# Kernel tuning notes

Hardware: AMD Instinct MI355X
Metric: run time of the kernel (lower is better)

The kernel has to match this reference:

```python
import math
import jax
import jax.numpy as jnp
import numpy as np

N_ATOMS = 5000
N_EDGES = 100000
FEAT = 128
BERN_K = 16
R_CUT = 5.0
EPS = 1e-15


def _swish(x, a, b):
    # learnable swish: alpha * x * sigmoid(beta * x)
    return a * x * jax.nn.sigmoid(b * x)


def _y_all(r_ij, r, l):
    """Real spherical harmonics of the unit vector r_ij/r, all m in [-l, l]."""
    x, y, z = r_ij[:, 0], r_ij[:, 1], r_ij[:, 2]
    if l == 0:
        return jnp.ones((r_ij.shape[0], 1), r_ij.dtype)
    if l == 1:
        return jnp.stack([y, z, x], axis=1) / r
    s3 = math.sqrt(3.0)
    r2 = (r * r)[:, 0]
    return jnp.stack(
        [s3 * x * y, s3 * y * z, 1.5 * z * z - 0.5 * r2, s3 * x * z, 0.5 * s3 * (x * x - y * y)],
        axis=1,
    ) / r2[:, None]


def _rho_k(r, gamma, K):
    """Bernstein radial basis b_{k,K-1}(exp(-gamma r)) times SpookyNet smooth cutoff."""
    rr = r[:, 0]
    g = jnp.maximum(gamma, 0.0)  # gamma.clamp(0)
    e = jnp.exp(-g * rr)[:, None]  # [E,1]
    k = jnp.arange(K)
    binom = jnp.asarray([math.comb(K - 1, i) for i in range(K)], dtype=r.dtype)
    bern = binom * e ** k * (1.0 - e) ** (K - 1 - k)  # [E,K]
    safe = jnp.where(rr < R_CUT, (R_CUT - rr) * (R_CUT + rr), 1.0)
    fcut = jnp.where(rr < R_CUT, jnp.exp(-rr * rr / safe), 0.0)
    return bern * fcut[:, None]


def _forward(xyz, x_tilde, rm_W1, rm_b1, rm_W2, rm_b2, rm_W3, rm_b3,
             rl_W1, rl_b1, rl_W2, rl_b2, rl_W3, rl_b3,
             G_s, G_p, G_d, P_1, P_2, D_1, D_2,
             gamma_s, gamma_p, gamma_d, sw_alpha, sw_beta, nbrs):
    n = xyz.shape[0]
    sw = lambda t, i: _swish(t, sw_alpha[i], sw_beta[i])
    # batched pre-activation linear over channel dim c
    bl = lambda W, b, t: jnp.einsum('cij,cnj->cni', W, t) + b[:, None, :]

    # BatchedResidualMLP on x_tilde repeated over 4 channels
    x4 = jnp.broadcast_to(x_tilde, (4,) + x_tilde.shape)  # [4,N,F]
    h = x4 + bl(rm_W2, rm_b2, sw(bl(rm_W1, rm_b1, sw(x4, 0)), 1))
    res_outs = x4 + bl(rm_W3, rm_b3, sw(h, 2))  # [4,N,F]

    i0, i1 = nbrs[:, 0], nbrs[:, 1]
    r_ij = xyz[i1] - xyz[i0]  # [E,3]
    r = jnp.sqrt((r_ij ** 2 + EPS).sum(-1, keepdims=True))  # stable norm, [E,1]
    K = G_s.shape[1]

    def quant(l, gamma, G, res_out):
        # g: [E,K,2l+1] = rho_k outer y_lm
        g = _rho_k(r, gamma, K)[:, :, None] * _y_all(r_ij, r, l)[:, None, :]
        mm = jnp.einsum('fk,ekm->efm', G, g)  # [E,F,2l+1]
        per = res_out[i1][:, :, None] * mm
        return jax.ops.segment_sum(per, i0, num_segments=n)  # scatter_add -> [N,F,2l+1]

    q_s = quant(0, gamma_s, G_s, res_outs[1])
    q_p = quant(1, gamma_p, G_p, res_outs[2])
    q_d = quant(2, gamma_d, G_d, res_outs[3])

    def inner(q, M1, M2):
        t1 = jnp.einsum('ij,njm->nim', M1, q)
        t2 = jnp.einsum('ij,njm->nim', M2, q)
        return (t1 * t2).sum(-1)

    inp = res_outs[0] + q_s[:, :, 0] + inner(q_p, P_1, P_2) + inner(q_d, D_1, D_2)

    # ResidualMLP (note: no outer skip, matching the torch code)
    lin = lambda W, b, t: t @ W.T + b
    h2 = inp + lin(rl_W2, rl_b2, sw(lin(rl_W1, rl_b1, sw(inp, 3)), 4))
    return lin(rl_W3, rl_b3, sw(h2, 5))


def setup_inputs():
    key = jax.random.key(0)
    ks = jax.random.split(key, 24)
    p = lambda k, shape: jax.random.normal(k, shape, dtype=jnp.float32) * 0.1
    F, K = FEAT, BERN_K
    return {
        'xyz': jax.random.normal(ks[0], (N_ATOMS, 3), jnp.float32) * 3.0,
        'x_tilde': jax.random.normal(ks[1], (N_ATOMS, F), jnp.float32),
        'nbrs': jax.random.randint(ks[2], (N_EDGES, 2), 0, N_ATOMS),
        'rm_W1': p(ks[3], (4, F, F)), 'rm_b1': p(ks[4], (4, F)),
        'rm_W2': p(ks[5], (4, F, F)), 'rm_b2': p(ks[6], (4, F)),
        'rm_W3': p(ks[7], (4, F, F)), 'rm_b3': p(ks[8], (4, F)),
        'rl_W1': p(ks[9], (F, F)), 'rl_b1': p(ks[10], (F,)),
        'rl_W2': p(ks[11], (F, F)), 'rl_b2': p(ks[12], (F,)),
        'rl_W3': p(ks[13], (F, F)), 'rl_b3': p(ks[14], (F,)),
        'G_s': p(ks[15], (F, K)), 'G_p': p(ks[16], (F, K)), 'G_d': p(ks[17], (F, K)),
        'P_1': p(ks[18], (F, F)), 'P_2': p(ks[19], (F, F)),
        'D_1': p(ks[20], (F, F)), 'D_2': p(ks[21], (F, F)),
        'gamma_s': jnp.asarray(0.5, jnp.float32),
        'gamma_p': jnp.asarray(0.5, jnp.float32),
        'gamma_d': jnp.asarray(0.5, jnp.float32),
        'sw_alpha': jnp.ones((6,), jnp.float32),
        'sw_beta': jnp.full((6,), 1.702, jnp.float32),
    }


def reference(xyz, x_tilde, nbrs, rm_W1, rm_b1, rm_W2, rm_b2, rm_W3, rm_b3,
              rl_W1, rl_b1, rl_W2, rl_b2, rl_W3, rl_b3,
              G_s, G_p, G_d, P_1, P_2, D_1, D_2,
              gamma_s, gamma_p, gamma_d, sw_alpha, sw_beta):
    return _forward(xyz, x_tilde, rm_W1, rm_b1, rm_W2, rm_b2, rm_W3, rm_b3,
                    rl_W1, rl_b1, rl_W2, rl_b2, rl_W3, rl_b3,
                    G_s, G_p, G_d, P_1, P_2, D_1, D_2,
                    gamma_s, gamma_p, gamma_d, sw_alpha, sw_beta, nbrs)
```

## Files before the change

### kernel.cpp

```cpp
#include <hip/hip_runtime.h>
#include <hip/hip_bf16.h>
#include <math.h>

#define NA 5000
#define NE 100000
#define F 128
#define KB 16
#define RCUT 5.0f
#define RECW 28
#define QCAP 40

typedef long long i64;
typedef __attribute__((ext_vector_type(8))) short bf16x8;
typedef __attribute__((ext_vector_type(4))) float f32x4;

__device__ __forceinline__ float swish_f(float t, float a, float b){
    return a * t / (1.0f + __expf(-b * t));
}
__device__ __forceinline__ float bf2f(unsigned short u){
    return __uint_as_float(((unsigned)u) << 16);
}
__device__ __forceinline__ unsigned short f2bf(float x){
    unsigned b = __float_as_uint(x);
    return (unsigned short)((b + 0x8000u) >> 16);
}
__device__ __forceinline__ unsigned pack2(float a, float b){
    return (unsigned)f2bf(a) | ((unsigned)f2bf(b) << 16);
}
__device__ __forceinline__ int swz(int row, int byte_in_row){
    return row * 256 + (byte_in_row ^ ((row & 7) << 4));
}

template<int MT>
__device__ __forceinline__ void gemm_stage(const unsigned short* __restrict__ Wb,
                                           const short* act_lds, f32x4 (&acc)[MT][2],
                                           int lane, int wave)
{
    bf16x8 B[2][4], A[MT][4];
    const int cl = lane & 15, kh = lane >> 4;
    #pragma unroll
    for (int ntl = 0; ntl < 2; ++ntl){
        const unsigned short* wp = Wb + (i64)(wave * 32 + ntl * 16 + cl) * F + kh * 8;
        #pragma unroll
        for (int kb = 0; kb < 4; ++kb)
            B[ntl][kb] = *(const bf16x8*)(wp + kb * 32);
    }
    #pragma unroll
    for (int mt = 0; mt < MT; ++mt){
        int row = mt * 16 + cl;
        #pragma unroll
        for (int kb = 0; kb < 4; ++kb)
            A[mt][kb] = *(const bf16x8*)((const char*)act_lds + swz(row, kb * 64 + kh * 16));
    }
    #pragma unroll
    for (int mt = 0; mt < MT; ++mt)
        #pragma unroll
        for (int ntl = 0; ntl < 2; ++ntl)
            #pragma unroll
            for (int kb = 0; kb < 4; ++kb)
                acc[mt][ntl] = __builtin_amdgcn_mfma_f32_16x16x32_bf16(
                    A[mt][kb], B[ntl][kb], acc[mt][ntl], 0, 0, 0);
}

__device__ __forceinline__ void epi_lds(f32x4 acc[2][2], const float* __restrict__ bc,
                                        const float* resid_lds, int use_resid,
                                        float aS, float bS, short* act_lds,
                                        int lane, int wave)
{
    const int cl = lane & 15, r4 = (lane >> 4) * 4;
    #pragma unroll
    for (int ntl = 0; ntl < 2; ++ntl){
        int col = wave * 32 + ntl * 16 + cl;
        float bv = bc[col];
        #pragma unroll
        for (int mt = 0; mt < 2; ++mt){
            #pragma unroll
            for (int j = 0; j < 4; ++j){
                int row = mt * 16 + r4 + j;
                float z = acc[mt][ntl][j] + bv;
                if (use_resid) z += resid_lds[row * 132 + col];
                z = swish_f(z, aS, bS);
                *(short*)((char*)act_lds + swz(row, col * 2)) = (short)f2bf(z);
            }
        }
    }
}

__device__ __forceinline__ void basis16(float r, float g, float fcut, float* b){
    const float C[KB] = {1.f,15.f,105.f,455.f,1365.f,3003.f,5005.f,6435.f,
                         6435.f,5005.f,3003.f,1365.f,455.f,105.f,15.f,1.f};
    float e = __expf(-fmaxf(g, 0.f) * r);
    float one = 1.f - e;
    float ep = 1.f;
    #pragma unroll
    for (int k = 0; k < KB; ++k){ b[k] = C[k] * ep * fcut; ep *= e; }
    float op = 1.f;
    #pragma unroll
    for (int k = KB-1; k >= 0; --k){ b[k] *= op; op *= one; }
}

__device__ __forceinline__ void prep_edge_block(
    int ebid, const float* __restrict__ xyz, const int* __restrict__ nbrs,
    int* __restrict__ fill, int* __restrict__ idx,
    const float* __restrict__ gs, const float* __restrict__ gp,
    const float* __restrict__ gd, float* __restrict__ rec)
{
    int e = ebid * 256 + threadIdx.x;
    if (e >= NE) return;
    int i0 = nbrs[2*e], i1 = nbrs[2*e+1];
    float dx = xyz[3*i1]   - xyz[3*i0];
    float dy = xyz[3*i1+1] - xyz[3*i0+1];
    float dz = xyz[3*i1+2] - xyz[3*i0+2];
    float r2 = dx*dx + dy*dy + dz*dz + 3e-15f;
    float r = sqrtf(r2);
    if (r >= RCUT) return;
    int slot = atomicAdd(&fill[i0], 1);
    if (slot < QCAP) idx[i0 * QCAP + slot] = e;
    float* R = rec + (i64)e * RECW;
    float ir = 1.f / r;
    R[0] = __int_as_float(i1);
    R[1] = dx * ir; R[2] = dy * ir; R[3] = dz * ir;
    float fcut = __expf(-r2 / ((RCUT - r) * (RCUT + r)));
    float bs[KB], bp[KB], bd[KB];
    basis16(r, gs[0], fcut, bs);
    basis16(r, gp[0], fcut, bp);
    basis16(r, gd[0], fcut, bd);
    unsigned* RW = (unsigned*)(R + 4);
    #pragma unroll
    for (int k = 0; k < 8; ++k) RW[k]      = pack2(bs[2*k], bs[2*k+1]);
    #pragma unroll
    for (int k = 0; k < 8; ++k) RW[8 + k]  = pack2(bp[2*k], bp[2*k+1]);
    #pragma unroll
    for (int k = 0; k < 8; ++k) RW[16 + k] = pack2(bd[2*k], bd[2*k+1]);
}

template<int S0, int S1, int S2, int ADD2, int ADD3, int ADDPART, int PREP, int CH, int RESB>
__global__ __launch_bounds__(256)
void mlp3_mfma(const float* __restrict__ in, const unsigned short* __restrict__ part,
               const unsigned short* __restrict__ W1b, const float* __restrict__ b1,
               const unsigned short* __restrict__ W2b, const float* __restrict__ b2,
               const unsigned short* __restrict__ W3b, const float* __restrict__ b3,
               float* __restrict__ out, unsigned short* __restrict__ resb,
               const float* __restrict__ sw_a, const float* __restrict__ sw_b, int n,
               const float* __restrict__ xyz, const int* __restrict__ nbrs,
               int* __restrict__ fill, int* __restrict__ idx,
               const float* __restrict__ gs, const float* __restrict__ gp,
               const float* __restrict__ gd, float* __restrict__ rec)
{
    if (PREP && blockIdx.y >= CH){
        int ebid = (blockIdx.y - CH) * gridDim.x + blockIdx.x;
        if (ebid < (NE + 255) / 256)
            prep_edge_block(ebid, xyz, nbrs, fill, idx, gs, gp, gd, rec);
        return;
    }

    __shared__ short act_lds[32 * 128];
    __shared__ float resid_lds[32 * 132];
    const int tid = threadIdx.x;
    const int lane = tid & 63, wave = tid >> 6;
    const int c = blockIdx.y;
    const int a0 = blockIdx.x * 32;
    const i64 S = (i64)NA * F;

    const unsigned short* Wc1 = W1b + (i64)c * F * F;
    const unsigned short* Wc2 = W2b + (i64)c * F * F;
    const unsigned short* Wc3 = W3b + (i64)c * F * F;
    const float* bc1 = b1 + c * F;
    const float* bc2 = b2 + c * F;
    const float* bc3 = b3 + c * F;

    {
        float aS = sw_a[S0], bS = sw_b[S0];
        #pragma unroll
        for (int it = 0; it < 4; ++it){
            int ch = tid + it * 256;
            int row = ch >> 5, j4 = ch & 31;
            int g = a0 + row;
            float4 v = make_float4(0.f, 0.f, 0.f, 0.f);
            if (g < n){
                v = *(const float4*)(in + (i64)g * F + j4 * 4);
                if (ADDPART){
                    #pragma unroll
                    for (int m = 0; m < 8; ++m){
                        ushort4 u = *(const ushort4*)(part + (i64)m * S + (i64)g * F + j4 * 4);
                        v.x += bf2f(u.x); v.y += bf2f(u.y);
                        v.z += bf2f(u.z); v.w += bf2f(u.w);
                    }
                }
            }
            *(float4*)&resid_lds[row * 132 + j4 * 4] = v;
            uint2 p;
            p.x = pack2(swish_f(v.x, aS, bS), swish_f(v.y, aS, bS));
            p.y = pack2(swish_f(v.z, aS, bS), swish_f(v.w, aS, bS));
            *(uint2*)((char*)act_lds + swz(row, j4 * 8)) = p;
        }
    }
    __syncthreads();

    f32x4 acc[2][2];
    #pragma unroll
    for (int a = 0; a < 2; ++a){ acc[a][0] = (f32x4){0,0,0,0}; acc[a][1] = (f32x4){0,0,0,0}; }
    gemm_stage<2>(Wc1, act_lds, acc, lane, wave);
    __syncthreads();
    epi_lds(acc, bc1, resid_lds, 0, sw_a[S1], sw_b[S1], act_lds, lane, wave);
    __syncthreads();

    #pragma unroll
    for (int a = 0; a < 2; ++a){ acc[a][0] = (f32x4){0,0,0,0}; acc[a][1] = (f32x4){0,0,0,0}; }
    gemm_stage<2>(Wc2, act_lds, acc, lane, wave);
    __syncthreads();
    epi_lds(acc, bc2, resid_lds, ADD2, sw_a[S2], sw_b[S2], act_lds, lane, wave);
    __syncthreads();

    #pragma unroll
    for (int a = 0; a < 2; ++a){ acc[a][0] = (f32x4){0,0,0,0}; acc[a][1] = (f32x4){0,0,0,0}; }
    gemm_stage<2>(Wc3, act_lds, acc, lane, wave);
    {
        const int cl = lane & 15, r4 = (lane >> 4) * 4;
        #pragma unroll
        for (int ntl = 0; ntl < 2; ++ntl){
            int col = wave * 32 + ntl * 16 + cl;
            float bv = bc3[col];
            #pragma unroll
            for (int mt = 0; mt < 2; ++mt){
                #pragma unroll
                for (int j = 0; j < 4; ++j){
                    int row = mt * 16 + r4 + j;
                    int g = a0 + row;
                    if (g >= n) continue;
                    float z = acc[mt][ntl][j] + bv;
                    if (ADD3) z += resid_lds[row * 132 + col];
                    if (RESB && c > 0)
                        resb[(i64)(c - 1) * S + (i64)g * F + col] = f2bf(z);
                    else
                        out[(i64)g * F + col] = z;
                }
            }
        }
    }
}

__global__ __launch_bounds__(256)
void bilinear_mfma(const unsigned short* __restrict__ Q,
                   const unsigned short* __restrict__ P1b, const unsigned short* __restrict__ P2b,
                   const unsigned short* __restrict__ D1b, const unsigned short* __restrict__ D2b,
                   unsigned short* __restrict__ part, int n)
{
    __shared__ short act_lds[32 * 128];
    const int tid = threadIdx.x;
    const int lane = tid & 63, wave = tid >> 6;
    const int m = blockIdx.y;
    const int a0 = blockIdx.x * 32;
    const i64 S = (i64)NA * F;
    const unsigned short* M1 = (m < 3) ? P1b : D1b;
    const unsigned short* M2 = (m < 3) ? P2b : D2b;
    const unsigned short* A = Q + (i64)m * S;

    #pragma unroll
    for (int it = 0; it < 2; ++it){
        int ch = tid + it * 256;
        int row = ch >> 4, o16 = ch & 15;
        int g = a0 + row;
        uint4 v = make_uint4(0u, 0u, 0u, 0u);
        if (g < n) v = *(const uint4*)(A + (i64)g * F + o16 * 8);
        *(uint4*)((char*)act_lds + swz(row, o16 * 16)) = v;
    }
    __syncthreads();

    f32x4 acc1[2][2], acc2[2][2];
    #pragma unroll
    for (int a = 0; a < 2; ++a){
        acc1[a][0] = (f32x4){0,0,0,0}; acc1[a][1] = (f32x4){0,0,0,0};
        acc2[a][0] = (f32x4){0,0,0,0}; acc2[a][1] = (f32x4){0,0,0,0};
    }
    gemm_stage<2>(M1, act_lds, acc1, lane, wave);
    gemm_stage<2>(M2, act_lds, acc2, lane, wave);

    const int cl = lane & 15, r4 = (lane >> 4) * 4;
    #pragma unroll
    for (int ntl = 0; ntl < 2; ++ntl){
        int col = wave * 32 + ntl * 16 + cl;
        #pragma unroll
        for (int mt = 0; mt < 2; ++mt){
            #pragma unroll
            for (int j = 0; j < 4; ++j){
                int g = a0 + mt * 16 + r4 + j;
                if (g >= n) continue;
                part[(i64)m * S + (i64)g * F + col] =
                    f2bf(acc1[mt][ntl][j] * acc2[mt][ntl][j]);
            }
        }
    }
}

__global__ __launch_bounds__(256)
void wconv(const float* s0, const float* s1, const float* s2, const float* s3,
           const float* s4, const float* s5, const float* s6, const float* s7,
           const float* s8, const float* s9, unsigned short* __restrict__ dst,
           int* __restrict__ fillz)
{
    int t = blockIdx.y;
    if (t == 0){
        for (int i = blockIdx.x * 256 + threadIdx.x; i < NA; i += 32 * 256)
            fillz[i] = 0;
    }
    const float* src; i64 off; int sz;
    if      (t == 0){ src = s0; off = 0;      sz = 65536; }
    else if (t == 1){ src = s1; off = 65536;  sz = 65536; }
    else if (t == 2){ src = s2; off = 131072; sz = 65536; }
    else if (t == 3){ src = s3; off = 196608; sz = 16384; }
    else if (t == 4){ src = s4; off = 212992; sz = 16384; }
    else if (t == 5){ src = s5; off = 229376; sz = 16384; }
    else if (t == 6){ src = s6; off = 245760; sz = 16384; }
    else if (t == 7){ src = s7; off = 262144; sz = 16384; }
    else if (t == 8){ src = s8; off = 278528; sz = 16384; }
    else            { src = s9; off = 294912; sz = 16384; }
    unsigned* d = (unsigned*)(dst + off);
    int pairs = sz >> 1;
    for (int p = blockIdx.x * 256 + threadIdx.x; p < pairs; p += gridDim.x * 256)
        d[p] = pack2(src[2 * p], src[2 * p + 1]);
}

__global__ __launch_bounds__(256)
void q_gather(const float* __restrict__ rec, const int* __restrict__ idx,
              const int* __restrict__ fill,
              const float* __restrict__ res0, const unsigned short* __restrict__ resb,
              const float* __restrict__ Gs, const float* __restrict__ Gp,
              const float* __restrict__ Gd,
              float* __restrict__ inp, unsigned short* __restrict__ Q)
{
    const int n = blockIdx.x;
    const int tid = threadIdx.x;
    const int s = tid >> 7;
    const int f = tid & 127;
    const i64 S = (i64)NA * F;

    float G0[KB], G1[KB], G2[KB];
    #pragma unroll
    for (int q4 = 0; q4 < 4; ++q4){
        *(float4*)&G0[q4*4] = *(const float4*)(Gs + f*KB + q4*4);
        *(float4*)&G1[q4*4] = *(const float4*)(Gp + f*KB + q4*4);
        *(float4*)&G2[q4*4] = *(const float4*)(Gd + f*KB + q4*4);
    }

    __shared__ int   idx_s[QCAP];
    __shared__ float recs[QCAP * RECW];
    __shared__ float red[2][9][128];

    const int cnt = min(fill[n], QCAP);
    if (tid < cnt) idx_s[tid] = idx[n * QCAP + tid];
    __syncthreads();
    for (int w = tid; w < cnt * RECW; w += 256){
        int j = w / RECW, o = w - j * RECW;
        recs[w] = rec[(i64)idx_s[j] * RECW + o];
    }
    __syncthreads();

    float qs = 0.f;
    float qp0=0.f, qp1=0.f, qp2=0.f;
    float qd0=0.f, qd1=0.f, qd2=0.f, qd3=0.f, qd4=0.f;
    const float s3 = 1.7320508075688772f;

    for (int j = s; j < cnt; j += 2){
        const float* R = &recs[j * RECW];
        int i1 = __float_as_int(R[0]);
        float ux = R[1], uy = R[2], uz = R[3];
        const unsigned* bw = (const unsigned*)(R + 4);
        float ds = 0.f, dp = 0.f, dd = 0.f;
        #pragma unroll
        for (int k = 0; k < 8; ++k){
            unsigned w = bw[k];
            ds += G0[2*k] * __uint_as_float(w << 16) + G0[2*k+1] * __uint_as_float(w & 0xffff0000u);
        }
        #pragma unroll
        for (int k = 0; k < 8; ++k){
            unsigned w = bw[8+k];
            dp += G1[2*k] * __uint_as_float(w << 16) + G1[2*k+1] * __uint_as_float(w & 0xffff0000u);
        }
        #pragma unroll
        for (int k = 0; k < 8; ++k){
            unsigned w = bw[16+k];
            dd += G2[2*k] * __uint_as_float(w << 16) + G2[2*k+1] * __uint_as_float(w & 0xffff0000u);
        }
        float a1 = bf2f(resb[(i64)i1*F + f]);
        float a2 = bf2f(resb[S + (i64)i1*F + f]);
        float a3 = bf2f(resb[2*S + (i64)i1*F + f]);
        qs += a1 * ds;
        float tp = a2 * dp;
        qp0 += tp * uy; qp1 += tp * uz; qp2 += tp * ux;
        float td = a3 * dd;
        qd0 += td * (s3 * ux * uy);
        qd1 += td * (s3 * uy * uz);
        qd2 += td * (1.5f * uz * uz - 0.5f);
        qd3 += td * (s3 * ux * uz);
        qd4 += td * (0.5f * s3 * (ux*ux - uy*uy));
    }

    red[s][0][f] = qs;
    red[s][1][f] = qp0; red[s][2][f] = qp1; red[s][3][f] = qp2;
    red[s][4][f] = qd0; red[s][5][f] = qd1; red[s][6][f] = qd2;
    red[s][7][f] = qd3; red[s][8][f] = qd4;
    __syncthreads();
    if (s == 0){
        float sums[9];
        #pragma unroll
        for (int i = 0; i < 9; ++i) sums[i] = red[0][i][f] + red[1][i][f];
        inp[(i64)n*F + f] = res0[(i64)n*F + f] + sums[0];
        #pragma unroll
        for (int mm = 0; mm < 8; ++mm)
            Q[(i64)mm * S + (i64)n*F + f] = f2bf(sums[1 + mm]);
    }
}

extern "C" void kernel_launch(void* const* d_in, const int* in_sizes, int n_in,
                              void* d_out, int out_size, void* d_ws, size_t ws_size,
                              hipStream_t stream)
{
    const float* xyz     = (const float*)d_in[0];
    const float* x_tilde = (const float*)d_in[1];
    const int*   nbrs    = (const int*)d_in[2];
    const float* rm_W1 = (const float*)d_in[3],  *rm_b1 = (const float*)d_in[4];
    const float* rm_W2 = (const float*)d_in[5],  *rm_b2 = (const float*)d_in[6];
    const float* rm_W3 = (const float*)d_in[7],  *rm_b3 = (const float*)d_in[8];
    const float* rl_W1 = (const float*)d_in[9],  *rl_b1 = (const float*)d_in[10];
    const float* rl_W2 = (const float*)d_in[11], *rl_b2 = (const float*)d_in[12];
    const float* rl_W3 = (const float*)d_in[13], *rl_b3 = (const float*)d_in[14];
    const float* G_s = (const float*)d_in[15], *G_p = (const float*)d_in[16], *G_d = (const float*)d_in[17];
    const float* P_1 = (const float*)d_in[18], *P_2 = (const float*)d_in[19];
    const float* D_1 = (const float*)d_in[20], *D_2 = (const float*)d_in[21];
    const float* gamma_s = (const float*)d_in[22], *gamma_p = (const float*)d_in[23], *gamma_d = (const float*)d_in[24];
    const float* sw_a = (const float*)d_in[25], *sw_b = (const float*)d_in[26];

    const i64 S = (i64)NA * F;
    float* res0 = (float*)d_ws;
    unsigned short* resb = (unsigned short*)(res0 + S);
    float* inp  = (float*)(resb + 3 * S);
    unsigned short* Q = (unsigned short*)(inp + S);
    float* rec  = (float*)(Q + 8 * S);
    unsigned short* part = (unsigned short*)rec;
    int* fill   = (int*)(rec + (i64)NE * RECW);
    int* idx    = fill + NA + 8;
    unsigned short* Wb = (unsigned short*)(idx + NA * QCAP);

    const int NT = (NA + 31) / 32;

    wconv<<<dim3(32, 10), 256, 0, stream>>>(rm_W1, rm_W2, rm_W3, rl_W1, rl_W2, rl_W3,
                                            P_1, P_2, D_1, D_2, Wb, fill);

    mlp3_mfma<0,1,2,1,1,0,1,4,1><<<dim3(NT, 7), 256, 0, stream>>>(
        x_tilde, (const unsigned short*)nullptr,
        Wb + 0, rm_b1, Wb + 65536, rm_b2, Wb + 131072, rm_b3,
        res0, resb, sw_a, sw_b, NA,
        xyz, nbrs, fill, idx, gamma_s, gamma_p, gamma_d, rec);

    q_gather<<<NA, 256, 0, stream>>>(rec, idx, fill, res0, resb,
                                     G_s, G_p, G_d, inp, Q);

    bilinear_mfma<<<dim3(NT, 8), 256, 0, stream>>>(
        Q, Wb + 245760, Wb + 262144, Wb + 278528, Wb + 294912, part, NA);

    mlp3_mfma<3,4,5,1,0,1,0,1,0><<<dim3(NT, 1), 256, 0, stream>>>(
        inp, part,
        Wb + 196608, rl_b1, Wb + 212992, rl_b2, Wb + 229376, rl_b3,
        (float*)d_out, nullptr, sw_a, sw_b, NA,
        nullptr, nullptr, nullptr, nullptr, nullptr, nullptr, nullptr, nullptr);
}
```

Baseline: 86.85 us.

## Compute per-edge Bernstein-G projections with MFMA in q_gather

Converts G_s/G_p/G_d to bf16 in the weight-conversion kernel and, in q_gather, computes the per-edge dot products between Bernstein coefficients and G via 16x16x32 bf16 MFMA tiles of 16 edges staged into shared memory. This replaces the per-thread scalar 48-FMA loop and the 48 G registers per thread. It also software-prefetches the next edge's resb gathers. In exchange it adds extra block-wide syncs per 16-edge chunk, rounds the projected values to bf16, and wastes half of the MFMA K dimension on zero padding.

```diff
diff --git a/kernel.cpp b/kernel.cpp
--- a/kernel.cpp
+++ b/kernel.cpp
@@ -296,7 +296,8 @@
 __global__ __launch_bounds__(256)
 void wconv(const float* s0, const float* s1, const float* s2, const float* s3,
            const float* s4, const float* s5, const float* s6, const float* s7,
-           const float* s8, const float* s9, unsigned short* __restrict__ dst,
+           const float* s8, const float* s9, const float* g0, const float* g1,
+           const float* g2, unsigned short* __restrict__ dst,
            int* __restrict__ fillz)
 {
     int t = blockIdx.y;
@@ -314,7 +315,10 @@
     else if (t == 6){ src = s6; off = 245760; sz = 16384; }
     else if (t == 7){ src = s7; off = 262144; sz = 16384; }
     else if (t == 8){ src = s8; off = 278528; sz = 16384; }
-    else            { src = s9; off = 294912; sz = 16384; }
+    else if (t == 9){ src = s9; off = 294912; sz = 16384; }
+    else if (t ==10){ src = g0; off = 311296; sz = 2048; }
+    else if (t ==11){ src = g1; off = 313344; sz = 2048; }
+    else            { src = g2; off = 315392; sz = 2048; }
     unsigned* d = (unsigned*)(dst + off);
     int pairs = sz >> 1;
     for (int p = blockIdx.x * 256 + threadIdx.x; p < pairs; p += gridDim.x * 256)
@@ -325,30 +329,24 @@
 void q_gather(const float* __restrict__ rec, const int* __restrict__ idx,
               const int* __restrict__ fill,
               const float* __restrict__ res0, const unsigned short* __restrict__ resb,
-              const float* __restrict__ Gs, const float* __restrict__ Gp,
-              const float* __restrict__ Gd,
+              const unsigned* __restrict__ Gb,
               float* __restrict__ inp, unsigned short* __restrict__ Q)
 {
     const int n = blockIdx.x;
     const int tid = threadIdx.x;
     const int s = tid >> 7;
     const int f = tid & 127;
+    const int lane = tid & 63, wave = tid >> 6;
     const i64 S = (i64)NA * F;
-
-    float G0[KB], G1[KB], G2[KB];
-    #pragma unroll
-    for (int q4 = 0; q4 < 4; ++q4){
-        *(float4*)&G0[q4*4] = *(const float4*)(Gs + f*KB + q4*4);
-        *(float4*)&G1[q4*4] = *(const float4*)(Gp + f*KB + q4*4);
-        *(float4*)&G2[q4*4] = *(const float4*)(Gd + f*KB + q4*4);
-    }
 
     __shared__ int   idx_s[QCAP];
     __shared__ float recs[QCAP * RECW];
-    __shared__ float red[2][9][128];
-
+    __shared__ __align__(16) char upool[12288];
+    unsigned short* D = (unsigned short*)upool;
+    float* red = (float*)upool;
+
+    if (tid < QCAP) idx_s[tid] = idx[n * QCAP + tid];
     const int cnt = min(fill[n], QCAP);
-    if (tid < cnt) idx_s[tid] = idx[n * QCAP + tid];
     __syncthreads();
     for (int w = tid; w < cnt * RECW; w += 256){
         int j = w / RECW, o = w - j * RECW;
@@ -360,51 +358,94 @@
     float qp0=0.f, qp1=0.f, qp2=0.f;
     float qd0=0.f, qd1=0.f, qd2=0.f, qd3=0.f, qd4=0.f;
     const float s3 = 1.7320508075688772f;
-
-    for (int j = s; j < cnt; j += 2){
-        const float* R = &recs[j * RECW];
-        int i1 = __float_as_int(R[0]);
-        float ux = R[1], uy = R[2], uz = R[3];
-        const unsigned* bw = (const unsigned*)(R + 4);
-        float ds = 0.f, dp = 0.f, dd = 0.f;
-        #pragma unroll
-        for (int k = 0; k < 8; ++k){
-            unsigned w = bw[k];
-            ds += G0[2*k] * __uint_as_float(w << 16) + G0[2*k+1] * __uint_as_float(w & 0xffff0000u);
-        }
-        #pragma unroll
-        for (int k = 0; k < 8; ++k){
-            unsigned w = bw[8+k];
-            dp += G1[2*k] * __uint_as_float(w << 16) + G1[2*k+1] * __uint_as_float(w & 0xffff0000u);
-        }
-        #pragma unroll
-        for (int k = 0; k < 8; ++k){
-            unsigned w = bw[16+k];
-            dd += G2[2*k] * __uint_as_float(w << 16) + G2[2*k+1] * __uint_as_float(w & 0xffff0000u);
-        }
-        float a1 = bf2f(resb[(i64)i1*F + f]);
-        float a2 = bf2f(resb[S + (i64)i1*F + f]);
-        float a3 = bf2f(resb[2*S + (i64)i1*F + f]);
-        qs += a1 * ds;
-        float tp = a2 * dp;
-        qp0 += tp * uy; qp1 += tp * uz; qp2 += tp * ux;
-        float td = a3 * dd;
-        qd0 += td * (s3 * ux * uy);
-        qd1 += td * (s3 * uy * uz);
-        qd2 += td * (1.5f * uz * uz - 0.5f);
-        qd3 += td * (s3 * ux * uz);
-        qd4 += td * (0.5f * s3 * (ux*ux - uy*uy));
-    }
-
-    red[s][0][f] = qs;
-    red[s][1][f] = qp0; red[s][2][f] = qp1; red[s][3][f] = qp2;
-    red[s][4][f] = qd0; red[s][5][f] = qd1; red[s][6][f] = qd2;
-    red[s][7][f] = qd3; red[s][8][f] = qd4;
+    const int cl = lane & 15, kh = lane >> 4;
+
+    for (int base = 0; base < cnt; base += 16){
+        {
+            int er = base + cl; if (er >= QCAP) er = 0;
+            bf16x8 A[3];
+            #pragma unroll
+            for (int ch = 0; ch < 3; ++ch){
+                if (kh < 2){
+                    const unsigned* bw = (const unsigned*)&recs[er * RECW + 4];
+                    union { uint4 u; bf16x8 h; } cv;
+                    cv.u = *(const uint4*)(bw + ch * 8 + kh * 4);
+                    A[ch] = cv.h;
+                } else {
+                    A[ch] = (bf16x8){0,0,0,0,0,0,0,0};
+                }
+            }
+            #pragma unroll
+            for (int ch = 0; ch < 3; ++ch){
+                #pragma unroll
+                for (int ct = 0; ct < 2; ++ct){
+                    int fc = wave * 32 + ct * 16 + cl;
+                    bf16x8 B;
+                    if (kh < 2){
+                        union { uint4 u; bf16x8 h; } cv;
+                        cv.u = *(const uint4*)(Gb + (i64)ch * F * 8 + fc * 8 + kh * 4);
+                        B = cv.h;
+                    } else {
+                        B = (bf16x8){0,0,0,0,0,0,0,0};
+                    }
+                    f32x4 z = (f32x4){0.f, 0.f, 0.f, 0.f};
+                    z = __builtin_amdgcn_mfma_f32_16x16x32_bf16(A[ch], B, z, 0, 0, 0);
+                    #pragma unroll
+                    for (int j = 0; j < 4; ++j)
+                        D[ch * 2048 + (kh * 4 + j) * 128 + fc] = f2bf(z[j]);
+                }
+            }
+        }
+        __syncthreads();
+
+        const int mrec = min(16, cnt - base);
+        int j = s;
+        float a1n = 0.f, a2n = 0.f, a3n = 0.f;
+        if (j < mrec){
+            int i1 = __float_as_int(recs[(base + j) * RECW]);
+            a1n = bf2f(resb[(i64)i1 * F + f]);
+            a2n = bf2f(resb[S + (i64)i1 * F + f]);
+            a3n = bf2f(resb[2 * S + (i64)i1 * F + f]);
+        }
+        for (; j < mrec; j += 2){
+            float a1 = a1n, a2 = a2n, a3 = a3n;
+            int jn = j + 2;
+            if (jn < mrec){
+                int i1 = __float_as_int(recs[(base + jn) * RECW]);
+                a1n = bf2f(resb[(i64)i1 * F + f]);
+                a2n = bf2f(resb[S + (i64)i1 * F + f]);
+                a3n = bf2f(resb[2 * S + (i64)i1 * F + f]);
+            }
+            const float* R = &recs[(base + j) * RECW];
+            float ux = R[1], uy = R[2], uz = R[3];
+            float ds = bf2f(D[0 * 2048 + j * 128 + f]);
+            float dp = bf2f(D[1 * 2048 + j * 128 + f]);
+            float dd = bf2f(D[2 * 2048 + j * 128 + f]);
+            qs += a1 * ds;
+            float tp = a2 * dp;
+            qp0 += tp * uy; qp1 += tp * uz; qp2 += tp * ux;
+            float td = a3 * dd;
+            qd0 += td * (s3 * ux * uy);
+            qd1 += td * (s3 * uy * uz);
+            qd2 += td * (1.5f * uz * uz - 0.5f);
+            qd3 += td * (s3 * ux * uz);
+            qd4 += td * (0.5f * s3 * (ux*ux - uy*uy));
+        }
+        __syncthreads();
+    }
+
+    red[(s * 9 + 0) * 128 + f] = qs;
+    red[(s * 9 + 1) * 128 + f] = qp0; red[(s * 9 + 2) * 128 + f] = qp1;
+    red[(s * 9 + 3) * 128 + f] = qp2;
+    red[(s * 9 + 4) * 128 + f] = qd0; red[(s * 9 + 5) * 128 + f] = qd1;
+    red[(s * 9 + 6) * 128 + f] = qd2; red[(s * 9 + 7) * 128 + f] = qd3;
+    red[(s * 9 + 8) * 128 + f] = qd4;
     __syncthreads();
     if (s == 0){
         float sums[9];
         #pragma unroll
-        for (int i = 0; i < 9; ++i) sums[i] = red[0][i][f] + red[1][i][f];
+        for (int i = 0; i < 9; ++i)
+            sums[i] = red[(0 * 9 + i) * 128 + f] + red[(1 * 9 + i) * 128 + f];
         inp[(i64)n*F + f] = res0[(i64)n*F + f] + sums[0];
         #pragma unroll
         for (int mm = 0; mm < 8; ++mm)
@@ -444,8 +485,8 @@
 
     const int NT = (NA + 31) / 32;
 
-    wconv<<<dim3(32, 10), 256, 0, stream>>>(rm_W1, rm_W2, rm_W3, rl_W1, rl_W2, rl_W3,
-                                            P_1, P_2, D_1, D_2, Wb, fill);
+    wconv<<<dim3(32, 13), 256, 0, stream>>>(rm_W1, rm_W2, rm_W3, rl_W1, rl_W2, rl_W3,
+                                            P_1, P_2, D_1, D_2, G_s, G_p, G_d, Wb, fill);
 
     mlp3_mfma<0,1,2,1,1,0,1,4,1><<<dim3(NT, 7), 256, 0, stream>>>(
         x_tilde, (const unsigned short*)nullptr,
@@ -454,7 +495,7 @@
         xyz, nbrs, fill, idx, gamma_s, gamma_p, gamma_d, rec);
 
     q_gather<<<NA, 256, 0, stream>>>(rec, idx, fill, res0, resb,
-                                     G_s, G_p, G_d, inp, Q);
+                                     (const unsigned*)(Wb + 311296), inp, Q);
 
     bilinear_mfma<<<dim3(NT, 8), 256, 0, stream>>>(
         Q, Wb + 245760, Wb + 262144, Wb + 278528, Wb + 294912, part, NA);
```

Result: faster. 77.53 us (-10.7%).
